# Optimization experiments

Hardware: AMD Instinct MI355X
Metric: run time of the kernel (lower is better)

The kernel has to match this reference:

```python
import jax, jax.numpy as jnp
import numpy as np

N_BLADES = 8
GRADE = np.array([0, 1, 1, 1, 2, 2, 2, 3])
WEIGHT_EXPANSION = np.array([0, 1, 1, 1, 2, 2, 2, 3])
GRADE_BLADES = ([0], [1, 2, 3], [4, 5, 6], [7])
EPS = 1e-6


def _build_cayley():
    # Blades as bitmasks over generators e1,e2,e3; canonical order = sorted by (grade, mask)
    # -> [1, e1, e2, e3, e12, e13, e23, e123], matching weight_expansion [0,1,1,1,2,2,2,3].
    masks = sorted(range(8), key=lambda m: (bin(m).count('1'), m))
    m2i = {m: i for i, m in enumerate(masks)}
    ti, tj, tk, ts, triples = [], [], [], [], []
    for i, a in enumerate(masks):
        for j, b in enumerate(masks):
            # reorder sign for Euclidean Cl(3,0): count transpositions
            swaps = sum(bin(a >> (bit + 1)).count('1') for bit in range(3) if (b >> bit) & 1)
            k = m2i[a ^ b]
            ti.append(i); tj.append(j); tk.append(k)
            ts.append(-1.0 if swaps % 2 else 1.0)
            triples.append((int(GRADE[i]), int(GRADE[j]), int(GRADE[k])))
    uniq = sorted(set(triples))  # 20 directed grade-interaction paths for P3M0
    pidx = {t: p for p, t in enumerate(uniq)}
    tp = np.array([pidx[t] for t in triples])
    return (np.array(ti), np.array(tj), np.array(tk),
            np.array(ts, dtype=np.float32), tp, len(uniq))


TI, TJ, TK, TS, TP, NUM_PATHS = _build_cayley()  # NUM_PATHS == 20


def _forward(x, linear_weight, linear_bias, gp_weight, normalize=True):
    # grade-wise linear map via blade-expanded weights: y[k] = x[k] @ W[grade(k)] + b
    y = jnp.einsum('kbi,kio->kbo', x, linear_weight[WEIGHT_EXPANSION]) + linear_bias
    y = jax.nn.gelu(y, approximate=True)
    # steerable weighted geometric product: one learnable weight per feature per grade path
    wpath = gp_weight.T[TP]  # [64, F]: path weight for each blade-product term
    terms = (TS[:, None, None] * wpath[:, None, :]) * x[TI] * y[TJ]  # [64, B, F]
    out = jax.ops.segment_sum(terms, TK, num_segments=N_BLADES)  # [8, B, F]
    if normalize:
        # grade-wise RMS norm: per sample, normalize each grade subspace over its blades and features
        parts = []
        for blades in GRADE_BLADES:
            og = out[np.array(blades)]  # [n_blades_g, B, F]
            rms = jnp.sqrt(jnp.mean(og * og, axis=(0, 2), keepdims=True) + EPS)
            parts.append(og / rms)
        out = jnp.concatenate(parts, axis=0)
    return out


def setup_inputs() -> dict:
    key = jax.random.key(0)
    k1, k2, k3 = jax.random.split(key, 3)
    B, F = 4096, 512
    x = jax.random.normal(k1, (N_BLADES, B, F), dtype=jnp.float32)
    gp_weight = jax.random.normal(k2, (F, NUM_PATHS), dtype=jnp.float32) * np.float32(1.0 / np.sqrt(3 + 1))
    linear_weight = jax.random.normal(k3, (4, F, F), dtype=jnp.float32) * np.float32(1.0 / np.sqrt(F))
    linear_bias = jnp.zeros((1, 1, F), dtype=jnp.float32)
    return {"x": x, "linear_weight": linear_weight, "linear_bias": linear_bias, "gp_weight": gp_weight}


def reference(x, linear_weight, linear_bias, gp_weight):
    return _forward(x, linear_weight, linear_bias, gp_weight, normalize=True)
```

## Files before the change

### kernel.cpp

```cpp
#include <hip/hip_runtime.h>

typedef short short8v __attribute__((ext_vector_type(8)));
typedef float f32x4 __attribute__((ext_vector_type(4)));
typedef unsigned short u16;
typedef unsigned int u32;

__device__ __forceinline__ u16 f2bf(float f) {
    u32 u = __float_as_uint(f);
    u += 0x7FFFu + ((u >> 16) & 1u);
    return (u16)(u >> 16);
}
__device__ __forceinline__ float bf2f(u16 h) {
    return __uint_as_float(((u32)h) << 16);
}
__device__ __forceinline__ float gelu_f(float v) {
    float u = 0.7978845608028654f * fmaf(0.044715f * v, v * v, v);
    return 0.5f * v * (1.0f + tanhf(u));
}
__device__ __forceinline__ void gload16(const void* g, void* l) {
    __builtin_amdgcn_global_load_lds(
        (const __attribute__((address_space(1))) u32*)g,
        (__attribute__((address_space(3))) u32*)l, 16, 0, 0);
}

__global__ __launch_bounds__(256) void k_cast_x(const float* __restrict__ x, u16* __restrict__ xb) {
    int idx = blockIdx.x * 256 + threadIdx.x;
    const float4* in = (const float4*)x;
    float4 a = in[idx * 2], c = in[idx * 2 + 1];
    short8v s;
    s[0] = (short)f2bf(a.x); s[1] = (short)f2bf(a.y); s[2] = (short)f2bf(a.z); s[3] = (short)f2bf(a.w);
    s[4] = (short)f2bf(c.x); s[5] = (short)f2bf(c.y); s[6] = (short)f2bf(c.z); s[7] = (short)f2bf(c.w);
    *(short8v*)(xb + (size_t)idx * 8) = s;
}

__global__ __launch_bounds__(1024) void k_prep_w(const float* __restrict__ w, u16* __restrict__ wt) {
    __shared__ float t[32][33];
    int g = blockIdx.z, o0 = blockIdx.x * 32, i0 = blockIdx.y * 32;
    int tx = threadIdx.x, ty = threadIdx.y;
    t[ty][tx] = w[(size_t)g * 262144 + (size_t)(i0 + ty) * 512 + (o0 + tx)];
    __syncthreads();
    wt[(size_t)g * 262144 + (size_t)(o0 + ty) * 512 + (i0 + tx)] = f2bf(t[tx][ty]);
}

__global__ __launch_bounds__(256) void k_prep_gp(const float* __restrict__ gp, float* __restrict__ gpt) {
    for (int l = threadIdx.x; l < 10240; l += 256) {
        int f = l / 20, p = l % 20;
        gpt[p * 512 + f] = gp[l];
    }
}

__global__ __launch_bounds__(256) void k_gemm(const u16* __restrict__ xb, const u16* __restrict__ wt,
                                              const float* __restrict__ bias, u16* __restrict__ yb) {
    __shared__ __align__(16) u16 sA[128 * 64];
    __shared__ __align__(16) u16 sB[128 * 64];
    const int tid = threadIdx.x;
    const int w = tid >> 6, lane = tid & 63;
    const int mt = blockIdx.x, nt = blockIdx.y;
    const int WE[8] = {0, 1, 1, 1, 2, 2, 2, 3};
    const int g = WE[mt >> 5];
    const u16* Abase = xb + (size_t)mt * 128 * 512;
    const u16* Bbase = wt + (size_t)g * 262144 + (size_t)nt * 128 * 512;
    const int wr = w >> 1, wc = w & 1;

    f32x4 acc[4][4];
#pragma unroll
    for (int m = 0; m < 4; m++)
#pragma unroll
        for (int n = 0; n < 4; n++) acc[m][n] = (f32x4){0.f, 0.f, 0.f, 0.f};

    const int lr = lane >> 3;
    const int lc = (lane & 7) * 16;
    for (int kt = 0; kt < 8; ++kt) {
#pragma unroll
        for (int p = 0; p < 4; ++p) {
            int chunk = w * 4 + p;
            const char* ga = (const char*)(Abase + ((size_t)(chunk * 8 + lr) * 512 + kt * 64)) + lc;
            gload16(ga, (char*)sA + chunk * 1024);
            const char* gb = (const char*)(Bbase + ((size_t)(chunk * 8 + lr) * 512 + kt * 64)) + lc;
            gload16(gb, (char*)sB + chunk * 1024);
        }
        __syncthreads();
#pragma unroll
        for (int kk = 0; kk < 2; ++kk) {
            short8v af[4], bf[4];
            const int ko = kk * 64 + ((lane >> 4) * 16);
#pragma unroll
            for (int m = 0; m < 4; m++) {
                int row = wr * 64 + m * 16 + (lane & 15);
                af[m] = *(const short8v*)((const char*)sA + row * 128 + ko);
            }
#pragma unroll
            for (int n = 0; n < 4; n++) {
                int col = wc * 64 + n * 16 + (lane & 15);
                bf[n] = *(const short8v*)((const char*)sB + col * 128 + ko);
            }
#pragma unroll
            for (int m = 0; m < 4; m++)
#pragma unroll
                for (int n = 0; n < 4; n++)
                    acc[m][n] = __builtin_amdgcn_mfma_f32_16x16x32_bf16(af[m], bf[n], acc[m][n], 0, 0, 0);
        }
        __syncthreads();
    }

    const size_t row0 = (size_t)mt * 128 + wr * 64;
    const int colBase = nt * 128 + wc * 64;
#pragma unroll
    for (int n = 0; n < 4; n++) {
        int col = colBase + n * 16 + (lane & 15);
        float bv = bias[col];
#pragma unroll
        for (int m = 0; m < 4; m++) {
#pragma unroll
            for (int j = 0; j < 4; j++) {
                size_t row = row0 + m * 16 + (lane >> 4) * 4 + j;
                float v = acc[m][n][j] + bv;
                yb[row * 512 + col] = f2bf(gelu_f(v));
            }
        }
    }
}

#define TERM(i, j, k, s, p) o[ff][k] = fmaf(s * wp[ff][p], xv[ff][i] * yv[ff][j], o[ff][k]);
#define GP_ALL \
    TERM(0,0,0, 1.0f,0) TERM(0,1,1, 1.0f,1) TERM(0,2,2, 1.0f,1) TERM(0,3,3, 1.0f,1) \
    TERM(0,4,4, 1.0f,2) TERM(0,5,5, 1.0f,2) TERM(0,6,6, 1.0f,2) TERM(0,7,7, 1.0f,3) \
    TERM(1,0,1, 1.0f,4) TERM(1,1,0, 1.0f,5) TERM(1,2,4, 1.0f,6) TERM(1,3,5, 1.0f,6) \
    TERM(1,4,2, 1.0f,7) TERM(1,5,3, 1.0f,7) TERM(1,6,7, 1.0f,8) TERM(1,7,6, 1.0f,9) \
    TERM(2,0,2, 1.0f,4) TERM(2,1,4,-1.0f,6) TERM(2,2,0, 1.0f,5) TERM(2,3,6, 1.0f,6) \
    TERM(2,4,1,-1.0f,7) TERM(2,5,7,-1.0f,8) TERM(2,6,3, 1.0f,7) TERM(2,7,5,-1.0f,9) \
    TERM(3,0,3, 1.0f,4) TERM(3,1,5,-1.0f,6) TERM(3,2,6,-1.0f,6) TERM(3,3,0, 1.0f,5) \
    TERM(3,4,7, 1.0f,8) TERM(3,5,1,-1.0f,7) TERM(3,6,2,-1.0f,7) TERM(3,7,4, 1.0f,9) \
    TERM(4,0,4, 1.0f,10) TERM(4,1,2,-1.0f,11) TERM(4,2,1, 1.0f,11) TERM(4,3,7, 1.0f,12) \
    TERM(4,4,0,-1.0f,13) TERM(4,5,6,-1.0f,14) TERM(4,6,5, 1.0f,14) TERM(4,7,3,-1.0f,15) \
    TERM(5,0,5, 1.0f,10) TERM(5,1,3,-1.0f,11) TERM(5,2,7,-1.0f,12) TERM(5,3,1, 1.0f,11) \
    TERM(5,4,6, 1.0f,14) TERM(5,5,0,-1.0f,13) TERM(5,6,4,-1.0f,14) TERM(5,7,2, 1.0f,15) \
    TERM(6,0,6, 1.0f,10) TERM(6,1,7, 1.0f,12) TERM(6,2,3,-1.0f,11) TERM(6,3,2, 1.0f,11) \
    TERM(6,4,5,-1.0f,14) TERM(6,5,4, 1.0f,14) TERM(6,6,0,-1.0f,13) TERM(6,7,1,-1.0f,15) \
    TERM(7,0,7, 1.0f,16) TERM(7,1,6, 1.0f,17) TERM(7,2,5,-1.0f,17) TERM(7,3,4, 1.0f,17) \
    TERM(7,4,3,-1.0f,18) TERM(7,5,2, 1.0f,18) TERM(7,6,1,-1.0f,18) TERM(7,7,0,-1.0f,19)

__global__ __launch_bounds__(256) void k_gp(const u16* __restrict__ xb, const u16* __restrict__ yb,
                                            const float* __restrict__ gpt, float* __restrict__ out) {
    const int b = blockIdx.x, tid = threadIdx.x;
    const int w = tid >> 6, lane = tid & 63;
    const int f0 = tid * 2;

    float xv[2][8], yv[2][8], wp[2][20], o[2][8];
#pragma unroll
    for (int i = 0; i < 8; i++) {
        u32 ux = *(const u32*)(xb + ((size_t)i * 4096 + b) * 512 + f0);
        xv[0][i] = bf2f((u16)(ux & 0xFFFF)); xv[1][i] = bf2f((u16)(ux >> 16));
        u32 uy = *(const u32*)(yb + ((size_t)i * 4096 + b) * 512 + f0);
        yv[0][i] = bf2f((u16)(uy & 0xFFFF)); yv[1][i] = bf2f((u16)(uy >> 16));
    }
#pragma unroll
    for (int p = 0; p < 20; p++) {
        float2 wv = *(const float2*)(gpt + p * 512 + f0);
        wp[0][p] = wv.x; wp[1][p] = wv.y;
    }

    float ss[4] = {0.f, 0.f, 0.f, 0.f};
#pragma unroll
    for (int ff = 0; ff < 2; ++ff) {
#pragma unroll
        for (int k = 0; k < 8; k++) o[ff][k] = 0.f;
        GP_ALL
        ss[0] += o[ff][0] * o[ff][0];
        ss[1] += o[ff][1] * o[ff][1] + o[ff][2] * o[ff][2] + o[ff][3] * o[ff][3];
        ss[2] += o[ff][4] * o[ff][4] + o[ff][5] * o[ff][5] + o[ff][6] * o[ff][6];
        ss[3] += o[ff][7] * o[ff][7];
    }

#pragma unroll
    for (int g2 = 0; g2 < 4; g2++) {
        float v = ss[g2];
#pragma unroll
        for (int off = 32; off >= 1; off >>= 1) v += __shfl_xor(v, off);
        ss[g2] = v;
    }
    __shared__ float red[4][4];
    if (lane == 0) { red[w][0] = ss[0]; red[w][1] = ss[1]; red[w][2] = ss[2]; red[w][3] = ss[3]; }
    __syncthreads();
    float inv[4];
    const float cnt[4] = {512.f, 1536.f, 1536.f, 512.f};
#pragma unroll
    for (int g2 = 0; g2 < 4; g2++) {
        float tot = red[0][g2] + red[1][g2] + red[2][g2] + red[3][g2];
        inv[g2] = 1.0f / sqrtf(tot / cnt[g2] + 1e-6f);
    }
    const int GK[8] = {0, 1, 1, 1, 2, 2, 2, 3};
#pragma unroll
    for (int k = 0; k < 8; k++) {
        float2 st;
        st.x = o[0][k] * inv[GK[k]];
        st.y = o[1][k] * inv[GK[k]];
        *(float2*)(out + ((size_t)k * 4096 + b) * 512 + f0) = st;
    }
}

extern "C" void kernel_launch(void* const* d_in, const int* in_sizes, int n_in,
                              void* d_out, int out_size, void* d_ws, size_t ws_size,
                              hipStream_t stream) {
    const float* x  = (const float*)d_in[0];
    const float* lw = (const float*)d_in[1];
    const float* lb = (const float*)d_in[2];
    const float* gp = (const float*)d_in[3];
    float* out = (float*)d_out;
    char* ws = (char*)d_ws;
    u16*   xb  = (u16*)ws;
    u16*   wt  = (u16*)(ws + 33554432);
    float* gpt = (float*)(ws + 35651584);
    u16*   yb  = (u16*)(ws + 35692544);

    hipLaunchKernelGGL(k_cast_x, dim3(8192), dim3(256), 0, stream, x, xb);
    hipLaunchKernelGGL(k_prep_w, dim3(16, 16, 4), dim3(32, 32), 0, stream, lw, wt);
    hipLaunchKernelGGL(k_prep_gp, dim3(1), dim3(256), 0, stream, gp, gpt);
    hipLaunchKernelGGL(k_gemm, dim3(256, 4), dim3(256), 0, stream, xb, wt, lb, yb);
    hipLaunchKernelGGL(k_gp, dim3(4096), dim3(256), 0, stream, xb, yb, gpt, out);
}
```

Measured before the change: 204.5 us.

## Merge prep kernels, double-buffer GEMM LDS, swizzle tiles, read gp weights directly

Merges the x cast and weight transpose into one launch and removes the gp transpose kernel. k_gp now reads gp weights in their original [F,20] layout with float4 loads. The GEMM gets double-buffered LDS so the next K-tile load overlaps the MFMA work, plus a block-index swizzle for better L2 reuse. Risks are higher LDS use, which lowers occupancy, and uncoalesced gp reads.

New measurement: 197.7 us. 1.03x faster.

```diff
diff --git a/kernel.cpp b/kernel.cpp
--- a/kernel.cpp
+++ b/kernel.cpp
@@ -23,85 +23,108 @@
         (__attribute__((address_space(3))) u32*)l, 16, 0, 0);
 }
 
-__global__ __launch_bounds__(256) void k_cast_x(const float* __restrict__ x, u16* __restrict__ xb) {
-    int idx = blockIdx.x * 256 + threadIdx.x;
-    const float4* in = (const float4*)x;
-    float4 a = in[idx * 2], c = in[idx * 2 + 1];
-    short8v s;
-    s[0] = (short)f2bf(a.x); s[1] = (short)f2bf(a.y); s[2] = (short)f2bf(a.z); s[3] = (short)f2bf(a.w);
-    s[4] = (short)f2bf(c.x); s[5] = (short)f2bf(c.y); s[6] = (short)f2bf(c.z); s[7] = (short)f2bf(c.w);
-    *(short8v*)(xb + (size_t)idx * 8) = s;
-}
-
-__global__ __launch_bounds__(1024) void k_prep_w(const float* __restrict__ w, u16* __restrict__ wt) {
-    __shared__ float t[32][33];
-    int g = blockIdx.z, o0 = blockIdx.x * 32, i0 = blockIdx.y * 32;
-    int tx = threadIdx.x, ty = threadIdx.y;
-    t[ty][tx] = w[(size_t)g * 262144 + (size_t)(i0 + ty) * 512 + (o0 + tx)];
-    __syncthreads();
-    wt[(size_t)g * 262144 + (size_t)(o0 + ty) * 512 + (i0 + tx)] = f2bf(t[tx][ty]);
-}
-
-__global__ __launch_bounds__(256) void k_prep_gp(const float* __restrict__ gp, float* __restrict__ gpt) {
-    for (int l = threadIdx.x; l < 10240; l += 256) {
-        int f = l / 20, p = l % 20;
-        gpt[p * 512 + f] = gp[l];
+__global__ __launch_bounds__(256) void k_prep(const float* __restrict__ x, u16* __restrict__ xb,
+                                              const float* __restrict__ w, u16* __restrict__ wt) {
+    const int bid = blockIdx.x, tid = threadIdx.x;
+    if (bid < 8192) {
+        int idx = bid * 256 + tid;
+        const float4* in = (const float4*)x;
+        float4 a = in[idx * 2], c = in[idx * 2 + 1];
+        short8v s;
+        s[0] = (short)f2bf(a.x); s[1] = (short)f2bf(a.y); s[2] = (short)f2bf(a.z); s[3] = (short)f2bf(a.w);
+        s[4] = (short)f2bf(c.x); s[5] = (short)f2bf(c.y); s[6] = (short)f2bf(c.z); s[7] = (short)f2bf(c.w);
+        *(short8v*)(xb + (size_t)idx * 8) = s;
+    } else {
+        __shared__ float t[32][33];
+        int tb = bid - 8192;
+        int g = tb >> 8, rem = tb & 255;
+        int o0 = (rem & 15) * 32, i0 = (rem >> 4) * 32;
+        int tx = tid & 31, ty4 = tid >> 5;
+#pragma unroll
+        for (int r = 0; r < 4; r++) {
+            int ty = ty4 * 4 + r;
+            t[ty][tx] = w[(size_t)g * 262144 + (size_t)(i0 + ty) * 512 + (o0 + tx)];
+        }
+        __syncthreads();
+#pragma unroll
+        for (int r = 0; r < 4; r++) {
+            int ty = ty4 * 4 + r;
+            wt[(size_t)g * 262144 + (size_t)(o0 + ty) * 512 + (i0 + tx)] = f2bf(t[tx][ty]);
+        }
     }
 }
 
 __global__ __launch_bounds__(256) void k_gemm(const u16* __restrict__ xb, const u16* __restrict__ wt,
                                               const float* __restrict__ bias, u16* __restrict__ yb) {
-    __shared__ __align__(16) u16 sA[128 * 64];
-    __shared__ __align__(16) u16 sB[128 * 64];
+    __shared__ __align__(16) u16 sA[2][128 * 64];
+    __shared__ __align__(16) u16 sB[2][128 * 64];
     const int tid = threadIdx.x;
     const int w = tid >> 6, lane = tid & 63;
-    const int mt = blockIdx.x, nt = blockIdx.y;
+    const int bid = blockIdx.x;
+    const int swz = (bid & 7) * 128 + (bid >> 3);
+    const int mt = swz >> 2, nt = swz & 3;
     const int WE[8] = {0, 1, 1, 1, 2, 2, 2, 3};
     const int g = WE[mt >> 5];
     const u16* Abase = xb + (size_t)mt * 128 * 512;
     const u16* Bbase = wt + (size_t)g * 262144 + (size_t)nt * 128 * 512;
     const int wr = w >> 1, wc = w & 1;
-
-    f32x4 acc[4][4];
-#pragma unroll
-    for (int m = 0; m < 4; m++)
-#pragma unroll
-        for (int n = 0; n < 4; n++) acc[m][n] = (f32x4){0.f, 0.f, 0.f, 0.f};
-
     const int lr = lane >> 3;
     const int lc = (lane & 7) * 16;
-    for (int kt = 0; kt < 8; ++kt) {
-#pragma unroll
-        for (int p = 0; p < 4; ++p) {
-            int chunk = w * 4 + p;
-            const char* ga = (const char*)(Abase + ((size_t)(chunk * 8 + lr) * 512 + kt * 64)) + lc;
-            gload16(ga, (char*)sA + chunk * 1024);
-            const char* gb = (const char*)(Bbase + ((size_t)(chunk * 8 + lr) * 512 + kt * 64)) + lc;
-            gload16(gb, (char*)sB + chunk * 1024);
-        }
+
+    f32x4 acc[4][4];
+#pragma unroll
+    for (int m = 0; m < 4; m++)
+#pragma unroll
+        for (int n = 0; n < 4; n++) acc[m][n] = (f32x4){0.f, 0.f, 0.f, 0.f};
+
+#define STAGE(BUF, KT) { \
+    _Pragma("unroll") \
+    for (int p = 0; p < 4; ++p) { \
+        int chunk = w * 4 + p; \
+        gload16((const char*)(Abase + ((size_t)(chunk * 8 + lr) * 512 + (KT) * 64)) + lc, \
+                (char*)sA[BUF] + chunk * 1024); \
+        gload16((const char*)(Bbase + ((size_t)(chunk * 8 + lr) * 512 + (KT) * 64)) + lc, \
+                (char*)sB[BUF] + chunk * 1024); \
+    } }
+
+#define COMPUTE(BUF) { \
+    _Pragma("unroll") \
+    for (int kk = 0; kk < 2; ++kk) { \
+        short8v af[4], bfr[4]; \
+        const int ko = kk * 64 + ((lane >> 4) * 16); \
+        _Pragma("unroll") \
+        for (int m = 0; m < 4; m++) { \
+            int row = wr * 64 + m * 16 + (lane & 15); \
+            af[m] = *(const short8v*)((const char*)sA[BUF] + row * 128 + ko); \
+        } \
+        _Pragma("unroll") \
+        for (int n = 0; n < 4; n++) { \
+            int col = wc * 64 + n * 16 + (lane & 15); \
+            bfr[n] = *(const short8v*)((const char*)sB[BUF] + col * 128 + ko); \
+        } \
+        _Pragma("unroll") \
+        for (int m = 0; m < 4; m++) \
+            _Pragma("unroll") \
+            for (int n = 0; n < 4; n++) \
+                acc[m][n] = __builtin_amdgcn_mfma_f32_16x16x32_bf16(af[m], bfr[n], acc[m][n], 0, 0, 0); \
+    } }
+
+    STAGE(0, 0);
+    __syncthreads();
+    for (int kt = 0; kt < 6; kt += 2) {
+        STAGE(1, kt + 1);
+        COMPUTE(0);
         __syncthreads();
-#pragma unroll
-        for (int kk = 0; kk < 2; ++kk) {
-            short8v af[4], bf[4];
-            const int ko = kk * 64 + ((lane >> 4) * 16);
-#pragma unroll
-            for (int m = 0; m < 4; m++) {
-                int row = wr * 64 + m * 16 + (lane & 15);
-                af[m] = *(const short8v*)((const char*)sA + row * 128 + ko);
-            }
-#pragma unroll
-            for (int n = 0; n < 4; n++) {
-                int col = wc * 64 + n * 16 + (lane & 15);
-                bf[n] = *(const short8v*)((const char*)sB + col * 128 + ko);
-            }
-#pragma unroll
-            for (int m = 0; m < 4; m++)
-#pragma unroll
-                for (int n = 0; n < 4; n++)
-                    acc[m][n] = __builtin_amdgcn_mfma_f32_16x16x32_bf16(af[m], bf[n], acc[m][n], 0, 0, 0);
-        }
+        STAGE(0, kt + 2);
+        COMPUTE(1);
         __syncthreads();
     }
+    STAGE(1, 7);
+    COMPUTE(0);
+    __syncthreads();
+    COMPUTE(1);
+#undef STAGE
+#undef COMPUTE
 
     const size_t row0 = (size_t)mt * 128 + wr * 64;
     const int colBase = nt * 128 + wc * 64;
@@ -141,7 +164,7 @@
     TERM(7,4,3,-1.0f,18) TERM(7,5,2, 1.0f,18) TERM(7,6,1,-1.0f,18) TERM(7,7,0,-1.0f,19)
 
 __global__ __launch_bounds__(256) void k_gp(const u16* __restrict__ xb, const u16* __restrict__ yb,
-                                            const float* __restrict__ gpt, float* __restrict__ out) {
+                                            const float* __restrict__ gp, float* __restrict__ out) {
     const int b = blockIdx.x, tid = threadIdx.x;
     const int w = tid >> 6, lane = tid & 63;
     const int f0 = tid * 2;
@@ -155,9 +178,14 @@
         yv[0][i] = bf2f((u16)(uy & 0xFFFF)); yv[1][i] = bf2f((u16)(uy >> 16));
     }
 #pragma unroll
-    for (int p = 0; p < 20; p++) {
-        float2 wv = *(const float2*)(gpt + p * 512 + f0);
-        wp[0][p] = wv.x; wp[1][p] = wv.y;
+    for (int ff = 0; ff < 2; ++ff) {
+        const float4* gv = (const float4*)(gp + (size_t)(f0 + ff) * 20);
+#pragma unroll
+        for (int q = 0; q < 5; ++q) {
+            float4 v = gv[q];
+            wp[ff][q * 4 + 0] = v.x; wp[ff][q * 4 + 1] = v.y;
+            wp[ff][q * 4 + 2] = v.z; wp[ff][q * 4 + 3] = v.w;
+        }
     }
 
     float ss[4] = {0.f, 0.f, 0.f, 0.f};
@@ -208,14 +236,11 @@
     const float* gp = (const float*)d_in[3];
     float* out = (float*)d_out;
     char* ws = (char*)d_ws;
-    u16*   xb  = (u16*)ws;
-    u16*   wt  = (u16*)(ws + 33554432);
-    float* gpt = (float*)(ws + 35651584);
-    u16*   yb  = (u16*)(ws + 35692544);
-
-    hipLaunchKernelGGL(k_cast_x, dim3(8192), dim3(256), 0, stream, x, xb);
-    hipLaunchKernelGGL(k_prep_w, dim3(16, 16, 4), dim3(32, 32), 0, stream, lw, wt);
-    hipLaunchKernelGGL(k_prep_gp, dim3(1), dim3(256), 0, stream, gp, gpt);
-    hipLaunchKernelGGL(k_gemm, dim3(256, 4), dim3(256), 0, stream, xb, wt, lb, yb);
-    hipLaunchKernelGGL(k_gp, dim3(4096), dim3(256), 0, stream, xb, yb, gpt, out);
-}
+    u16* xb = (u16*)ws;
+    u16* wt = (u16*)(ws + 33554432);
+    u16* yb = (u16*)(ws + 35651584);
+
+    hipLaunchKernelGGL(k_prep, dim3(9216), dim3(256), 0, stream, x, xb, lw, wt);
+    hipLaunchKernelGGL(k_gemm, dim3(1024), dim3(256), 0, stream, xb, wt, lb, yb);
+    hipLaunchKernelGGL(k_gp, dim3(4096), dim3(256), 0, stream, xb, yb, gp, out);
+}
```
